# Kernel optimization log

Measured on AMD Instinct MI355X. Metric: run time of the kernel, lower is better.

The kernel has to match this reference:

```python
import jax, jax.numpy as jnp
import numpy as np

B, L, H, NH = 32, 512, 256, 4
DH = H // NH
EPS = 1e-12


def setup_inputs() -> dict:
    key = jax.random.key(0)
    ks = jax.random.split(key, 24)
    p = lambda k, shape: 0.02 * jax.random.normal(k, shape, dtype=jnp.float32)
    return {
        "input_tensor": jax.random.normal(ks[0], (B, L, H), dtype=jnp.float32),
        # sorted positive timestamps (seconds-like scale)
        "time_seq": jnp.sort(jax.random.uniform(ks[1], (B, L), dtype=jnp.float32) * 100.0, axis=-1),
        "attention_mask": jnp.zeros((B, 1, L, L), dtype=jnp.float32),
        "item_seq_len": jnp.clip(jax.random.randint(ks[2], (B,), 0, L), 2, L),
        "Wq": p(ks[3], (H, H)), "bq": jnp.zeros((H,), jnp.float32),
        "Wk": p(ks[4], (H, H)), "bk": jnp.zeros((H,), jnp.float32),
        "Wv": p(ks[5], (H, H)), "bv": jnp.zeros((H,), jnp.float32),
        "Wd": p(ks[6], (H, H)), "bd": jnp.zeros((H,), jnp.float32),
        "ln_g": jnp.ones((H,), jnp.float32), "ln_b": jnp.zeros((H,), jnp.float32),
        "Wtq": p(ks[7], (H, H)), "btq": jnp.zeros((H,), jnp.float32),
        "tw1": p(ks[8], (L, L)), "tb1": p(ks[9], (L, L)),
        "tow1": p(ks[10], (L, L)), "tow2": p(ks[11], (L, L)), "tob": p(ks[12], (L, L)),
        "Wt": p(ks[13], (1, 2 * H)), "bt": jnp.zeros((1,), jnp.float32),
    }


def reference(input_tensor, time_seq, attention_mask, item_seq_len,
              Wq, bq, Wk, bk, Wv, bv, Wd, bd, ln_g, ln_b,
              Wtq, btq, tw1, tb1, tow1, tow2, tob, Wt, bt):
    x = input_tensor  # (B, L, H)

    def heads(t):  # (B,L,H) -> (B,NH,L,DH)
        return t.reshape(B, L, NH, DH).transpose(0, 2, 1, 3)

    q = heads(x @ Wq.T + bq)
    k = heads(x @ Wk.T + bk)
    v = heads(x @ Wv.T + bv)

    scores = jnp.einsum('bhqd,bhkd->bhqk', q, k)  # (B,NH,L,L)

    # --- time decay gate ---
    tq = x @ Wtq.T + btq                                  # (B,L,H)
    time_query_key = jnp.tanh(jnp.einsum('bqh,bkh->bqk', tq, x))  # (B,L,L)
    diff = jnp.abs(time_seq[:, :, None] - time_seq[:, None, :])   # |t_i - t_j|
    decay = jnp.tanh(jnp.log1p(diff) * tw1 + tb1)
    decay_gate = tow1 * decay + tow2 * time_query_key + tob       # (B,L,L)
    time_attn = jax.nn.sigmoid(decay_gate)[:, None, :, :]         # (B,1,L,L)

    scores = scores * time_attn / jnp.sqrt(jnp.float32(DH)) + attention_mask
    probs = jax.nn.softmax(scores, axis=-1)

    ctx = jnp.einsum('bhqk,bhkd->bhqd', probs, v)
    ctx = ctx.transpose(0, 2, 1, 3).reshape(B, L, H)

    hs = ctx @ Wd.T + bd + x
    mu = jnp.mean(hs, axis=-1, keepdims=True)
    var = jnp.var(hs, axis=-1, keepdims=True)
    hs = (hs - mu) / jnp.sqrt(var + EPS) * ln_g + ln_b   # (B,L,H)

    bidx = jnp.arange(B)
    emb1 = hs[bidx, item_seq_len - 1]  # (B,H)
    emb2 = hs[bidx, item_seq_len - 2]  # (B,H)
    pred_intervals = jnp.concatenate([emb1, emb2], axis=1) @ Wt.T + bt  # (B,1)
    return hs, pred_intervals
```

## Files before the change

kernel.cpp:

```cpp
#include <hip/hip_runtime.h>
#include <math.h>

#define Bn 32
#define Ln 512
#define Hn 256
#define NHn 4
#define DHn 64

typedef __attribute__((ext_vector_type(8))) short bf16x8;
typedef __attribute__((ext_vector_type(4))) float f32x4;
typedef unsigned int uint32;

__device__ __forceinline__ short f2b(float f) {
    union { float f; uint32 u; } v; v.f = f;
    uint32 r = (v.u + 0x7FFFu + ((v.u >> 16) & 1u)) >> 16;
    return (short)r;
}
__device__ __forceinline__ float b2f(short h) {
    union { uint32 u; float f; } v; v.u = ((uint32)(unsigned short)h) << 16;
    return v.f;
}
__device__ __forceinline__ float fast_tanh(float x) {
    float e = __expf(2.f * x);
    return 1.f - 2.f * __builtin_amdgcn_rcpf(e + 1.f);
}
__device__ __forceinline__ float fast_sigmoid(float x) {
    return __builtin_amdgcn_rcpf(1.f + __expf(-x));
}

__global__ __launch_bounds__(256) void conv_kernel(
    const float* __restrict__ x,
    const float* __restrict__ Wq, const float* __restrict__ Wk,
    const float* __restrict__ Wv, const float* __restrict__ Wtq,
    const float* __restrict__ Wd,
    short* __restrict__ xb, short* __restrict__ wb)
{
    const size_t NLH = (size_t)Bn * Ln * Hn;
    size_t i4 = ((size_t)blockIdx.x * 256 + threadIdx.x) * 4;
    if (i4 < NLH) {
        float4 v = *(const float4*)(x + i4);
        short4 o; o.x = f2b(v.x); o.y = f2b(v.y); o.z = f2b(v.z); o.w = f2b(v.w);
        *(short4*)(xb + i4) = o;
    } else {
        size_t off = i4 - NLH;
        int w = (int)(off >> 16);
        size_t wi = off & 65535;
        const float* src = (w == 0) ? Wq : (w == 1) ? Wk : (w == 2) ? Wv : (w == 3) ? Wtq : Wd;
        float4 v = *(const float4*)(src + wi);
        short4 o; o.x = f2b(v.x); o.y = f2b(v.y); o.z = f2b(v.z); o.w = f2b(v.w);
        *(short4*)(wb + off) = o;
    }
}

struct Acc { f32x4 t[4]; };

__device__ __forceinline__ void gemm_tile_64(
    const short* __restrict__ A,
    const short* __restrict__ Bm,
    int K, short* As, short* Bs, Acc& acc)
{
    const int tid = threadIdx.x;
    const int lane = tid & 63, w = tid >> 6;
    const int quad = lane >> 4, lm = lane & 15;
    const int srow = tid >> 3;
    const int slot = tid & 7;

    for (int k0 = 0; k0 < K; k0 += 64) {
        __syncthreads();
#pragma unroll
        for (int iss = 0; iss < 2; ++iss) {
            int r = srow + iss * 32;
            bf16x8 av = *(const bf16x8*)(A + (size_t)r * K + k0 + slot * 8);
            bf16x8 bv = *(const bf16x8*)(Bm + (size_t)r * K + k0 + slot * 8);
            *(bf16x8*)(As + r * 72 + slot * 8) = av;
            *(bf16x8*)(Bs + r * 72 + slot * 8) = bv;
        }
        __syncthreads();
#pragma unroll
        for (int ks = 0; ks < 2; ++ks) {
            bf16x8 a = *(const bf16x8*)(As + (w * 16 + lm) * 72 + ks * 32 + quad * 8);
#pragma unroll
            for (int kt = 0; kt < 4; ++kt) {
                bf16x8 b = *(const bf16x8*)(Bs + (kt * 16 + lm) * 72 + ks * 32 + quad * 8);
                acc.t[kt] = __builtin_amdgcn_mfma_f32_16x16x32_bf16(a, b, acc.t[kt], 0, 0, 0);
            }
        }
    }
}

__global__ __launch_bounds__(256) void proj_kernel(
    const short* __restrict__ xb, const short* __restrict__ wb,
    const float* __restrict__ bq, const float* __restrict__ bk,
    const float* __restrict__ bv, const float* __restrict__ btq,
    short* __restrict__ qb, short* __restrict__ kb,
    short* __restrict__ vb, short* __restrict__ tqb)
{
    __shared__ short As[64 * 72];
    __shared__ short Bs[64 * 72];
    const int tensor = blockIdx.x >> 2;
    const int ncol0 = (blockIdx.x & 3) * 64;
    const int m0 = blockIdx.y * 64;
    const short* A = xb + (size_t)m0 * Hn;
    const short* Bw = wb + (size_t)tensor * 65536 + (size_t)ncol0 * Hn;
    const float* bias = (tensor == 0) ? bq : (tensor == 1) ? bk : (tensor == 2) ? bv : btq;
    short* out = (tensor == 0) ? qb : (tensor == 1) ? kb : (tensor == 2) ? vb : tqb;

    Acc acc;
#pragma unroll
    for (int i = 0; i < 4; ++i) acc.t[i] = (f32x4){0.f, 0.f, 0.f, 0.f};
    gemm_tile_64(A, Bw, Hn, As, Bs, acc);

    const int lane = threadIdx.x & 63, w = threadIdx.x >> 6;
    const int quad = lane >> 4, lm = lane & 15;
#pragma unroll
    for (int kt = 0; kt < 4; ++kt) {
        int n = ncol0 + kt * 16 + lm;
        float bs = bias[n];
#pragma unroll
        for (int r = 0; r < 4; ++r) {
            int row = m0 + w * 16 + quad * 4 + r;
            out[(size_t)row * Hn + n] = f2b(acc.t[kt][r] + bs);
        }
    }
}

__global__ __launch_bounds__(256) void gate_kernel(
    const short* __restrict__ tqb, const short* __restrict__ xb,
    const float* __restrict__ tseq,
    const float* __restrict__ tw1, const float* __restrict__ tb1,
    const float* __restrict__ tow1, const float* __restrict__ tow2,
    const float* __restrict__ tob,
    short* __restrict__ gateb)
{
    __shared__ short As[64 * 72];
    __shared__ short Bs[64 * 72];
    const int b = blockIdx.z;
    const int m0 = blockIdx.y * 64, n0 = blockIdx.x * 64;
    const short* A = tqb + ((size_t)b * Ln + m0) * Hn;
    const short* Bw = xb + ((size_t)b * Ln + n0) * Hn;

    Acc acc;
#pragma unroll
    for (int i = 0; i < 4; ++i) acc.t[i] = (f32x4){0.f, 0.f, 0.f, 0.f};
    gemm_tile_64(A, Bw, Hn, As, Bs, acc);

    const int lane = threadIdx.x & 63, w = threadIdx.x >> 6;
    const int quad = lane >> 4, lm = lane & 15;
    const float* ts = tseq + (size_t)b * Ln;
    float ti[4];
#pragma unroll
    for (int r = 0; r < 4; ++r) ti[r] = ts[m0 + w * 16 + quad * 4 + r];
#pragma unroll
    for (int kt = 0; kt < 4; ++kt) {
        int j = n0 + kt * 16 + lm;
        float tj = ts[j];
#pragma unroll
        for (int r = 0; r < 4; ++r) {
            int i = m0 + w * 16 + quad * 4 + r;
            size_t ij = (size_t)i * Ln + j;
            float lg = __logf(1.f + fabsf(ti[r] - tj));
            float dec = fast_tanh(lg * tw1[ij] + tb1[ij]);
            float tqk = fast_tanh(acc.t[kt][r]);
            float dg = tow1[ij] * dec + tow2[ij] * tqk + tob[ij];
            float g = 0.125f * fast_sigmoid(dg);
            gateb[(size_t)b * Ln * Ln + ij] = f2b(g);
        }
    }
}

__global__ __launch_bounds__(256) void flash_mfma(
    const short* __restrict__ qb, const short* __restrict__ kb,
    const short* __restrict__ vb, const short* __restrict__ gateb,
    const float* __restrict__ mask, short* __restrict__ ctxb)
{
    __shared__ short Ks[64 * 72];
    __shared__ short Vt[64 * 72];
    __shared__ short Ps[4 * 16 * 72];
    const int q0 = blockIdx.x * 64;
    const int h = blockIdx.y, b = blockIdx.z;
    const int tid = threadIdx.x;
    const int w = tid >> 6, lane = tid & 63;
    const int quad = lane >> 4, lm = lane & 15;

    bf16x8 qf0, qf1;
    {
        const short* qrow = qb + ((size_t)(b * Ln + q0 + w * 16 + lm)) * Hn + h * DHn;
        qf0 = *(const bf16x8*)(qrow + quad * 8);
        qf1 = *(const bf16x8*)(qrow + 32 + quad * 8);
    }

    f32x4 o[4];
#pragma unroll
    for (int i = 0; i < 4; ++i) o[i] = (f32x4){0.f, 0.f, 0.f, 0.f};
    float m_run[4] = {-INFINITY, -INFINITY, -INFINITY, -INFINITY};
    float l_run[4] = {0.f, 0.f, 0.f, 0.f};
    const short* gr_base = gateb + (size_t)b * Ln * Ln;
    const float* mk_base = mask + (size_t)b * Ln * Ln;
    const int qrow0 = q0 + w * 16 + quad * 4;

    for (int k0 = 0; k0 < Ln; k0 += 64) {
        __syncthreads();
        {
            int srow = tid >> 3, slot = tid & 7;
#pragma unroll
            for (int iss = 0; iss < 2; ++iss) {
                int r = srow + iss * 32;
                bf16x8 kv = *(const bf16x8*)(kb + ((size_t)(b * Ln + k0 + r)) * Hn + h * DHn + slot * 8);
                *(bf16x8*)(Ks + r * 72 + slot * 8) = kv;
            }
        }
        {
            int key = tid >> 2, dq = tid & 3;
            const short* vr = vb + ((size_t)(b * Ln + k0 + key)) * Hn + h * DHn + dq * 16;
            bf16x8 v0 = *(const bf16x8*)(vr);
            bf16x8 v1 = *(const bf16x8*)(vr + 8);
#pragma unroll
            for (int u = 0; u < 8; ++u) Vt[(dq * 16 + u) * 72 + key] = v0[u];
#pragma unroll
            for (int u = 0; u < 8; ++u) Vt[(dq * 16 + 8 + u) * 72 + key] = v1[u];
        }
        __syncthreads();

        f32x4 s[4];
#pragma unroll
        for (int kt = 0; kt < 4; ++kt) {
            s[kt] = (f32x4){0.f, 0.f, 0.f, 0.f};
            bf16x8 b0 = *(const bf16x8*)(Ks + (kt * 16 + lm) * 72 + quad * 8);
            s[kt] = __builtin_amdgcn_mfma_f32_16x16x32_bf16(qf0, b0, s[kt], 0, 0, 0);
            bf16x8 b1 = *(const bf16x8*)(Ks + (kt * 16 + lm) * 72 + 32 + quad * 8);
            s[kt] = __builtin_amdgcn_mfma_f32_16x16x32_bf16(qf1, b1, s[kt], 0, 0, 0);
        }

        float mnew[4];
#pragma unroll
        for (int r = 0; r < 4; ++r) mnew[r] = m_run[r];
#pragma unroll
        for (int kt = 0; kt < 4; ++kt) {
            int col = k0 + kt * 16 + lm;
#pragma unroll
            for (int r = 0; r < 4; ++r) {
                float g = b2f(gr_base[(size_t)(qrow0 + r) * Ln + col]);
                float mv = mk_base[(size_t)(qrow0 + r) * Ln + col];
                float sv = s[kt][r] * g + mv;
                s[kt][r] = sv;
                mnew[r] = fmaxf(mnew[r], sv);
            }
        }
        float alpha[4], rsum[4];
#pragma unroll
        for (int r = 0; r < 4; ++r) {
#pragma unroll
            for (int off = 1; off < 16; off <<= 1)
                mnew[r] = fmaxf(mnew[r], __shfl_xor(mnew[r], off, 64));
            alpha[r] = __expf(m_run[r] - mnew[r]);
            m_run[r] = mnew[r];
            rsum[r] = 0.f;
        }
        float p[4][4];
#pragma unroll
        for (int kt = 0; kt < 4; ++kt)
#pragma unroll
            for (int r = 0; r < 4; ++r) {
                float pv = __expf(s[kt][r] - m_run[r]);
                p[kt][r] = pv;
                rsum[r] += pv;
            }
#pragma unroll
        for (int r = 0; r < 4; ++r) {
#pragma unroll
            for (int off = 1; off < 16; off <<= 1) rsum[r] += __shfl_xor(rsum[r], off, 64);
            l_run[r] = l_run[r] * alpha[r] + rsum[r];
#pragma unroll
            for (int ot = 0; ot < 4; ++ot) o[ot][r] *= alpha[r];
        }
        short* pw = Ps + w * 16 * 72;
#pragma unroll
        for (int kt = 0; kt < 4; ++kt)
#pragma unroll
            for (int r = 0; r < 4; ++r)
                pw[(quad * 4 + r) * 72 + kt * 16 + lm] = f2b(p[kt][r]);

#pragma unroll
        for (int ks = 0; ks < 2; ++ks) {
            bf16x8 pa = *(const bf16x8*)(pw + lm * 72 + ks * 32 + quad * 8);
#pragma unroll
            for (int ot = 0; ot < 4; ++ot) {
                bf16x8 vv = *(const bf16x8*)(Vt + (ot * 16 + lm) * 72 + ks * 32 + quad * 8);
                o[ot] = __builtin_amdgcn_mfma_f32_16x16x32_bf16(pa, vv, o[ot], 0, 0, 0);
            }
        }
    }

    float inv[4];
#pragma unroll
    for (int r = 0; r < 4; ++r) inv[r] = 1.0f / l_run[r];
#pragma unroll
    for (int ot = 0; ot < 4; ++ot) {
        int d = h * DHn + ot * 16 + lm;
#pragma unroll
        for (int r = 0; r < 4; ++r) {
            int row = b * Ln + qrow0 + r;
            ctxb[(size_t)row * Hn + d] = f2b(o[ot][r] * inv[r]);
        }
    }
}

__global__ __launch_bounds__(256) void outproj_kernel(
    const short* __restrict__ ctxb, const short* __restrict__ wdb,
    const float* __restrict__ bd, const float* __restrict__ x,
    float* __restrict__ out)
{
    __shared__ short As[64 * 72];
    __shared__ short Bs[64 * 72];
    const int n0 = blockIdx.x * 64, m0 = blockIdx.y * 64;
    Acc acc;
#pragma unroll
    for (int i = 0; i < 4; ++i) acc.t[i] = (f32x4){0.f, 0.f, 0.f, 0.f};
    gemm_tile_64(ctxb + (size_t)m0 * Hn, wdb + (size_t)n0 * Hn, Hn, As, Bs, acc);

    const int lane = threadIdx.x & 63, w = threadIdx.x >> 6;
    const int quad = lane >> 4, lm = lane & 15;
#pragma unroll
    for (int kt = 0; kt < 4; ++kt) {
        int n = n0 + kt * 16 + lm;
        float bs = bd[n];
#pragma unroll
        for (int r = 0; r < 4; ++r) {
            int row = m0 + w * 16 + quad * 4 + r;
            out[(size_t)row * Hn + n] = acc.t[kt][r] + bs + x[(size_t)row * Hn + n];
        }
    }
}

__global__ __launch_bounds__(256) void ln_kernel(float* __restrict__ hs,
                                                 const float* __restrict__ g,
                                                 const float* __restrict__ bta)
{
    const int row = blockIdx.x, t = threadIdx.x;
    float v = hs[(size_t)row * Hn + t];
    float s1 = v, s2 = v * v;
#pragma unroll
    for (int off = 32; off > 0; off >>= 1) {
        s1 += __shfl_xor(s1, off, 64);
        s2 += __shfl_xor(s2, off, 64);
    }
    __shared__ float red[8];
    if ((t & 63) == 0) { red[t >> 6] = s1; red[4 + (t >> 6)] = s2; }
    __syncthreads();
    float sum = red[0] + red[1] + red[2] + red[3];
    float sq  = red[4] + red[5] + red[6] + red[7];
    float mu  = sum * (1.f / 256.f);
    float var = sq * (1.f / 256.f) - mu * mu;
    float rstd = rsqrtf(var + 1e-12f);
    hs[(size_t)row * Hn + t] = (v - mu) * rstd * g[t] + bta[t];
}

__global__ __launch_bounds__(256) void pred_kernel(const float* __restrict__ hs,
                                                   const int* __restrict__ lens,
                                                   const float* __restrict__ Wt,
                                                   const float* __restrict__ bt,
                                                   float* __restrict__ pred)
{
    const int b = blockIdx.x, t = threadIdx.x;
    int len = lens[b];
    float e1 = hs[((size_t)b * Ln + (len - 1)) * Hn + t];
    float e2 = hs[((size_t)b * Ln + (len - 2)) * Hn + t];
    float v = e1 * Wt[t] + e2 * Wt[Hn + t];
#pragma unroll
    for (int off = 32; off > 0; off >>= 1) v += __shfl_xor(v, off, 64);
    __shared__ float ps[4];
    if ((t & 63) == 0) ps[t >> 6] = v;
    __syncthreads();
    if (t == 0) pred[b] = ps[0] + ps[1] + ps[2] + ps[3] + bt[0];
}

extern "C" void kernel_launch(void* const* d_in, const int* in_sizes, int n_in,
                              void* d_out, int out_size, void* d_ws, size_t ws_size,
                              hipStream_t stream) {
    (void)in_sizes; (void)n_in; (void)out_size; (void)ws_size;
    const float* x    = (const float*)d_in[0];
    const float* tseq = (const float*)d_in[1];
    const float* mask = (const float*)d_in[2];
    const int*   lens = (const int*)d_in[3];
    const float* Wq = (const float*)d_in[4];  const float* bq = (const float*)d_in[5];
    const float* Wk = (const float*)d_in[6];  const float* bk = (const float*)d_in[7];
    const float* Wv = (const float*)d_in[8];  const float* bv = (const float*)d_in[9];
    const float* Wd = (const float*)d_in[10]; const float* bd = (const float*)d_in[11];
    const float* ln_g = (const float*)d_in[12]; const float* ln_b = (const float*)d_in[13];
    const float* Wtq = (const float*)d_in[14]; const float* btq = (const float*)d_in[15];
    const float* tw1 = (const float*)d_in[16]; const float* tb1 = (const float*)d_in[17];
    const float* tow1 = (const float*)d_in[18]; const float* tow2 = (const float*)d_in[19];
    const float* tob = (const float*)d_in[20];
    const float* Wt = (const float*)d_in[21]; const float* bt = (const float*)d_in[22];

    const size_t NLH = (size_t)Bn * Ln * Hn;
    short* ws = (short*)d_ws;
    short* xb    = ws;
    short* wb    = xb + NLH;
    short* qb    = wb + 5 * 65536;
    short* kb    = qb + NLH;
    short* vb    = kb + NLH;
    short* tqb   = vb + NLH;
    short* gateb = tqb + NLH;
    short* ctxb  = gateb + (size_t)Bn * Ln * Ln;
    float* out   = (float*)d_out;

    dim3 blk(256);
    conv_kernel<<<dim3(4416), blk, 0, stream>>>(x, Wq, Wk, Wv, Wtq, Wd, xb, wb);
    proj_kernel<<<dim3(16, 256), blk, 0, stream>>>(xb, wb, bq, bk, bv, btq, qb, kb, vb, tqb);
    gate_kernel<<<dim3(8, 8, Bn), blk, 0, stream>>>(tqb, xb, tseq, tw1, tb1, tow1, tow2, tob, gateb);
    flash_mfma<<<dim3(8, NHn, Bn), blk, 0, stream>>>(qb, kb, vb, gateb, mask, ctxb);
    outproj_kernel<<<dim3(4, 256), blk, 0, stream>>>(ctxb, wb + 4 * 65536, bd, x, out);
    ln_kernel<<<dim3(Bn * Ln), blk, 0, stream>>>(out, ln_g, ln_b);
    pred_kernel<<<dim3(Bn), blk, 0, stream>>>(out, lens, Wt, bt, out + NLH);
}
```

Before: 238.5 us.

## Pack mask with gate as bf16 pair and pre-transpose V in projection

The gate kernel now reads the attention mask once and stores it as bf16 alongside the gate in one 32-bit word. The attention kernel then reads one packed word instead of a bf16 gate plus an fp32 mask for every head. The V projection is written in a per-head transposed layout, so the attention kernel loads V tiles with vector copies instead of scalar shared-memory transposes. The trade-offs are scattered 2-byte stores for V in the projection kernel, a larger gate buffer, and reduced mask precision.

Result: slower. 246.2 us (+3.2%).

```diff
diff --git a/kernel.cpp b/kernel.cpp
--- a/kernel.cpp
+++ b/kernel.cpp
@@ -93,7 +93,7 @@
     const float* __restrict__ bq, const float* __restrict__ bk,
     const float* __restrict__ bv, const float* __restrict__ btq,
     short* __restrict__ qb, short* __restrict__ kb,
-    short* __restrict__ vb, short* __restrict__ tqb)
+    short* __restrict__ vt, short* __restrict__ tqb)
 {
     __shared__ short As[64 * 72];
     __shared__ short Bs[64 * 72];
@@ -103,7 +103,6 @@
     const short* A = xb + (size_t)m0 * Hn;
     const short* Bw = wb + (size_t)tensor * 65536 + (size_t)ncol0 * Hn;
     const float* bias = (tensor == 0) ? bq : (tensor == 1) ? bk : (tensor == 2) ? bv : btq;
-    short* out = (tensor == 0) ? qb : (tensor == 1) ? kb : (tensor == 2) ? vb : tqb;
 
     Acc acc;
 #pragma unroll
@@ -112,14 +111,31 @@
 
     const int lane = threadIdx.x & 63, w = threadIdx.x >> 6;
     const int quad = lane >> 4, lm = lane & 15;
-#pragma unroll
-    for (int kt = 0; kt < 4; ++kt) {
-        int n = ncol0 + kt * 16 + lm;
-        float bs = bias[n];
-#pragma unroll
-        for (int r = 0; r < 4; ++r) {
-            int row = m0 + w * 16 + quad * 4 + r;
-            out[(size_t)row * Hn + n] = f2b(acc.t[kt][r] + bs);
+
+    if (tensor == 2) {
+#pragma unroll
+        for (int kt = 0; kt < 4; ++kt) {
+            int n = ncol0 + kt * 16 + lm;
+            float bs = bv[n];
+            int h = n >> 6, d = n & 63;
+#pragma unroll
+            for (int r = 0; r < 4; ++r) {
+                int row = m0 + w * 16 + quad * 4 + r;
+                int bb = row >> 9, l = row & 511;
+                vt[((size_t)(bb * NHn + h) * DHn + d) * Ln + l] = f2b(acc.t[kt][r] + bs);
+            }
+        }
+    } else {
+        short* out = (tensor == 0) ? qb : (tensor == 1) ? kb : tqb;
+#pragma unroll
+        for (int kt = 0; kt < 4; ++kt) {
+            int n = ncol0 + kt * 16 + lm;
+            float bs = bias[n];
+#pragma unroll
+            for (int r = 0; r < 4; ++r) {
+                int row = m0 + w * 16 + quad * 4 + r;
+                out[(size_t)row * Hn + n] = f2b(acc.t[kt][r] + bs);
+            }
         }
     }
 }
@@ -129,8 +145,8 @@
     const float* __restrict__ tseq,
     const float* __restrict__ tw1, const float* __restrict__ tb1,
     const float* __restrict__ tow1, const float* __restrict__ tow2,
-    const float* __restrict__ tob,
-    short* __restrict__ gateb)
+    const float* __restrict__ tob, const float* __restrict__ mask,
+    uint32* __restrict__ gateb)
 {
     __shared__ short As[64 * 72];
     __shared__ short Bs[64 * 72];
@@ -147,6 +163,8 @@
     const int lane = threadIdx.x & 63, w = threadIdx.x >> 6;
     const int quad = lane >> 4, lm = lane & 15;
     const float* ts = tseq + (size_t)b * Ln;
+    const float* mk = mask + (size_t)b * Ln * Ln;
+    uint32* go = gateb + (size_t)b * Ln * Ln;
     float ti[4];
 #pragma unroll
     for (int r = 0; r < 4; ++r) ti[r] = ts[m0 + w * 16 + quad * 4 + r];
@@ -163,15 +181,17 @@
             float tqk = fast_tanh(acc.t[kt][r]);
             float dg = tow1[ij] * dec + tow2[ij] * tqk + tob[ij];
             float g = 0.125f * fast_sigmoid(dg);
-            gateb[(size_t)b * Ln * Ln + ij] = f2b(g);
+            uint32 pk = ((uint32)(unsigned short)f2b(mk[ij]) << 16)
+                      |  (uint32)(unsigned short)f2b(g);
+            go[ij] = pk;
         }
     }
 }
 
 __global__ __launch_bounds__(256) void flash_mfma(
     const short* __restrict__ qb, const short* __restrict__ kb,
-    const short* __restrict__ vb, const short* __restrict__ gateb,
-    const float* __restrict__ mask, short* __restrict__ ctxb)
+    const short* __restrict__ vt, const uint32* __restrict__ gateb,
+    short* __restrict__ ctxb)
 {
     __shared__ short Ks[64 * 72];
     __shared__ short Vt[64 * 72];
@@ -194,9 +214,9 @@
     for (int i = 0; i < 4; ++i) o[i] = (f32x4){0.f, 0.f, 0.f, 0.f};
     float m_run[4] = {-INFINITY, -INFINITY, -INFINITY, -INFINITY};
     float l_run[4] = {0.f, 0.f, 0.f, 0.f};
-    const short* gr_base = gateb + (size_t)b * Ln * Ln;
-    const float* mk_base = mask + (size_t)b * Ln * Ln;
+    const uint32* gm_base = gateb + (size_t)b * Ln * Ln;
     const int qrow0 = q0 + w * 16 + quad * 4;
+    const short* vbase = vt + (size_t)(b * NHn + h) * DHn * Ln;
 
     for (int k0 = 0; k0 < Ln; k0 += 64) {
         __syncthreads();
@@ -207,17 +227,9 @@
                 int r = srow + iss * 32;
                 bf16x8 kv = *(const bf16x8*)(kb + ((size_t)(b * Ln + k0 + r)) * Hn + h * DHn + slot * 8);
                 *(bf16x8*)(Ks + r * 72 + slot * 8) = kv;
-            }
-        }
-        {
-            int key = tid >> 2, dq = tid & 3;
-            const short* vr = vb + ((size_t)(b * Ln + k0 + key)) * Hn + h * DHn + dq * 16;
-            bf16x8 v0 = *(const bf16x8*)(vr);
-            bf16x8 v1 = *(const bf16x8*)(vr + 8);
-#pragma unroll
-            for (int u = 0; u < 8; ++u) Vt[(dq * 16 + u) * 72 + key] = v0[u];
-#pragma unroll
-            for (int u = 0; u < 8; ++u) Vt[(dq * 16 + 8 + u) * 72 + key] = v1[u];
+                bf16x8 vv = *(const bf16x8*)(vbase + (size_t)r * Ln + k0 + slot * 8);
+                *(bf16x8*)(Vt + r * 72 + slot * 8) = vv;
+            }
         }
         __syncthreads();
 
@@ -239,8 +251,9 @@
             int col = k0 + kt * 16 + lm;
 #pragma unroll
             for (int r = 0; r < 4; ++r) {
-                float g = b2f(gr_base[(size_t)(qrow0 + r) * Ln + col]);
-                float mv = mk_base[(size_t)(qrow0 + r) * Ln + col];
+                uint32 gm = gm_base[(size_t)(qrow0 + r) * Ln + col];
+                float g  = b2f((short)(gm & 0xFFFFu));
+                float mv = b2f((short)(gm >> 16));
                 float sv = s[kt][r] * g + mv;
                 s[kt][r] = sv;
                 mnew[r] = fmaxf(mnew[r], sv);
@@ -399,17 +412,17 @@
     short* wb    = xb + NLH;
     short* qb    = wb + 5 * 65536;
     short* kb    = qb + NLH;
-    short* vb    = kb + NLH;
-    short* tqb   = vb + NLH;
-    short* gateb = tqb + NLH;
-    short* ctxb  = gateb + (size_t)Bn * Ln * Ln;
+    short* vt    = kb + NLH;
+    short* tqb   = vt + NLH;
+    uint32* gateb = (uint32*)(tqb + NLH);
+    short* ctxb  = tqb;
     float* out   = (float*)d_out;
 
     dim3 blk(256);
     conv_kernel<<<dim3(4416), blk, 0, stream>>>(x, Wq, Wk, Wv, Wtq, Wd, xb, wb);
-    proj_kernel<<<dim3(16, 256), blk, 0, stream>>>(xb, wb, bq, bk, bv, btq, qb, kb, vb, tqb);
-    gate_kernel<<<dim3(8, 8, Bn), blk, 0, stream>>>(tqb, xb, tseq, tw1, tb1, tow1, tow2, tob, gateb);
-    flash_mfma<<<dim3(8, NHn, Bn), blk, 0, stream>>>(qb, kb, vb, gateb, mask, ctxb);
+    proj_kernel<<<dim3(16, 256), blk, 0, stream>>>(xb, wb, bq, bk, bv, btq, qb, kb, vt, tqb);
+    gate_kernel<<<dim3(8, 8, Bn), blk, 0, stream>>>(tqb, xb, tseq, tw1, tb1, tow1, tow2, tob, mask, gateb);
+    flash_mfma<<<dim3(8, NHn, Bn), blk, 0, stream>>>(qb, kb, vt, gateb, ctxb);
     outproj_kernel<<<dim3(4, 256), blk, 0, stream>>>(ctxb, wb + 4 * 65536, bd, x, out);
     ln_kernel<<<dim3(Bn * Ln), blk, 0, stream>>>(out, ln_g, ln_b);
     pred_kernel<<<dim3(Bn), blk, 0, stream>>>(out, lens, Wt, bt, out + NLH);
```
